# Kernel optimization log

Measured on AMD Instinct MI355X. Metric: run time of the kernel, lower is better.

The kernel has to match this reference:

```python
import jax, jax.numpy as jnp
import numpy as np

PAD_ID = 50256  # GPT-J eos token used as pad


def setup_inputs() -> dict:
    key = jax.random.key(0)
    k1, k2, k3, k4 = jax.random.split(key, 4)
    B, S, D = 4, 2048, 4096  # B preference pairs -> 2B rows
    hidden_states = jax.random.normal(k1, (2 * B, S, D), dtype=jnp.float32)
    v_head_w = jax.random.normal(k2, (D,), dtype=jnp.float32) / np.sqrt(D).astype(np.float32)
    # tokens in [1, PAD_ID) so PAD only appears where we place it
    chosen = jax.random.randint(k3, (B, S), 1, PAD_ID)
    rejected = jax.random.randint(k4, (B, S), 1, PAD_ID)
    PROMPT = 512  # shared prompt so divergence_ind > 0
    rejected = rejected.at[:, :PROMPT].set(chosen[:, :PROMPT])
    pos = jnp.arange(S)[None, :]
    chosen = jnp.where(pos >= 1536, PAD_ID, chosen)     # chosen padded from 1536
    rejected = jnp.where(pos >= 1792, PAD_ID, rejected)  # rejected padded from 1792
    input_ids = jnp.concatenate([chosen, rejected], axis=0).astype(jnp.int64)
    return {"hidden_states": hidden_states, "v_head_w": v_head_w, "input_ids": input_ids}


def _first_index(mask, default):
    # index of first True along last axis, else `default`
    return jnp.where(mask.any(axis=-1), jnp.argmax(mask, axis=-1), default)


def reference(hidden_states, v_head_w, input_ids):
    # v_head: Linear(D, 1, bias=False) then squeeze(-1)
    rewards = jnp.einsum('bsd,d->bs', hidden_states, v_head_w)  # [2B, S]
    bs = input_ids.shape[0] // 2
    S = input_ids.shape[1]
    chosen, rejected = input_ids[:bs], input_ids[bs:]
    c_rew, r_rew = rewards[:bs], rewards[bs:]

    div_ind = _first_index(chosen != rejected, S)       # first divergence per pair
    c_ind = _first_index(chosen == PAD_ID, S)           # first pad (or S)
    r_ind = _first_index(rejected == PAD_ID, S)
    end_ind = jnp.maximum(c_ind, r_ind)

    pos = jnp.arange(S)[None, :]                         # [1, S]
    mask = (pos >= div_ind[:, None]) & (pos < end_ind[:, None])  # truncation window
    cnt = jnp.maximum(mask.sum(axis=-1), 1).astype(rewards.dtype)

    chosen_mean_scores = jnp.sum(jnp.where(mask, c_rew, 0.0), axis=-1) / cnt
    rejected_mean_scores = jnp.sum(jnp.where(mask, r_rew, 0.0), axis=-1) / cnt
    last = (end_ind - 1)[:, None]
    chosen_end_scores = jnp.take_along_axis(c_rew, last, axis=1)[:, 0]
    rejected_end_scores = jnp.take_along_axis(r_rew, last, axis=1)[:, 0]

    # -log(sigmoid(c - r)) averaged over the truncated window, then over pairs
    per_tok = -jax.nn.log_sigmoid(c_rew - r_rew)
    per_sample = jnp.sum(jnp.where(mask, per_tok, 0.0), axis=-1) / cnt
    loss = per_sample.mean()

    return loss, rewards, chosen_mean_scores, rejected_mean_scores, chosen_end_scores, rejected_end_scores
```

## Files before the change

### kernel.cpp

```cpp
#include <hip/hip_runtime.h>
#include <hip/hip_bf16.h>
#include <math.h>

#define PAD_ID 50256
#define S_LEN 2048
#define B_PAIRS 4
#define D4_C 1024
#define ROWS_PER_WAVE 2

__global__ __launch_bounds__(256) void rewards_kernel(
    const float4* __restrict__ hs,
    const float4* __restrict__ w4,
    float* __restrict__ rew,
    int nrows)
{
    const int wave = threadIdx.x >> 6;
    const int lane = threadIdx.x & 63;
    const int row0 = (blockIdx.x * 4 + wave) * ROWS_PER_WAVE;

    float4 wv[16];
    #pragma unroll
    for (int k = 0; k < 16; ++k)
        wv[k] = w4[lane + 64 * k];

    #pragma unroll
    for (int r = 0; r < ROWS_PER_WAVE; ++r) {
        const int row = row0 + r;
        if (row >= nrows) return;
        const float4* rp = hs + (size_t)row * D4_C;

        float acc0 = 0.0f, acc1 = 0.0f;
        #pragma unroll
        for (int k = 0; k < 16; k += 2) {
            float4 a0 = rp[lane + 64 * k];
            float4 a1 = rp[lane + 64 * (k + 1)];
            acc0 = fmaf(a0.x, wv[k].x, acc0);
            acc0 = fmaf(a0.y, wv[k].y, acc0);
            acc0 = fmaf(a0.z, wv[k].z, acc0);
            acc0 = fmaf(a0.w, wv[k].w, acc0);
            acc1 = fmaf(a1.x, wv[k + 1].x, acc1);
            acc1 = fmaf(a1.y, wv[k + 1].y, acc1);
            acc1 = fmaf(a1.z, wv[k + 1].z, acc1);
            acc1 = fmaf(a1.w, wv[k + 1].w, acc1);
        }
        float acc = acc0 + acc1;

        #pragma unroll
        for (int off = 32; off > 0; off >>= 1)
            acc += __shfl_down(acc, off, 64);
        if (lane == 0) rew[row] = acc;
    }
}

__device__ inline float wave_sum(float v) {
    #pragma unroll
    for (int off = 32; off > 0; off >>= 1) v += __shfl_down(v, off, 64);
    return v;
}
__device__ inline int wave_min(int v) {
    #pragma unroll
    for (int off = 32; off > 0; off >>= 1) v = min(v, __shfl_down(v, off, 64));
    return v;
}

__global__ __launch_bounds__(256) void scores_kernel(
    const float* __restrict__ rew,
    const int*   __restrict__ ids,
    float* __restrict__ out)
{
    __shared__ int   si[3][4];
    __shared__ float sf[3][4];
    __shared__ int   s_div, s_end;
    __shared__ float s_loss;

    const int tid  = threadIdx.x;
    const int lane = tid & 63;
    const int wave = tid >> 6;

    if (tid == 0) s_loss = 0.0f;
    __syncthreads();

    for (int b = 0; b < B_PAIRS; ++b) {
        const int*   ch = ids + (size_t)b * S_LEN;
        const int*   rj = ids + (size_t)(B_PAIRS + b) * S_LEN;
        const float* cr = rew + (size_t)b * S_LEN;
        const float* rr = rew + (size_t)(B_PAIRS + b) * S_LEN;

        int ldiv = S_LEN, lc = S_LEN, lr = S_LEN;
        for (int s = tid; s < S_LEN; s += 256) {
            int c = ch[s], r = rj[s];
            if (c != r)      ldiv = min(ldiv, s);
            if (c == PAD_ID) lc   = min(lc, s);
            if (r == PAD_ID) lr   = min(lr, s);
        }
        ldiv = wave_min(ldiv); lc = wave_min(lc); lr = wave_min(lr);
        if (lane == 0) { si[0][wave] = ldiv; si[1][wave] = lc; si[2][wave] = lr; }
        __syncthreads();
        if (tid == 0) {
            int dv = min(min(si[0][0], si[0][1]), min(si[0][2], si[0][3]));
            int ci = min(min(si[1][0], si[1][1]), min(si[1][2], si[1][3]));
            int ri = min(min(si[2][0], si[2][1]), min(si[2][2], si[2][3]));
            s_div = dv;
            s_end = max(ci, ri);
        }
        __syncthreads();
        const int dv = s_div, en = s_end;

        float sc = 0.0f, sr = 0.0f, sl = 0.0f;
        for (int s = dv + tid; s < en; s += 256) {
            float cv = cr[s], rv = rr[s];
            sc += cv;
            sr += rv;
            float x = cv - rv;
            sl += fmaxf(-x, 0.0f) + log1pf(expf(-fabsf(x)));
        }
        sc = wave_sum(sc); sr = wave_sum(sr); sl = wave_sum(sl);
        if (lane == 0) { sf[0][wave] = sc; sf[1][wave] = sr; sf[2][wave] = sl; }
        __syncthreads();
        if (tid == 0) {
            float tsc = sf[0][0] + sf[0][1] + sf[0][2] + sf[0][3];
            float tsr = sf[1][0] + sf[1][1] + sf[1][2] + sf[1][3];
            float tsl = sf[2][0] + sf[2][1] + sf[2][2] + sf[2][3];
            int cnt_i = en - dv;
            if (cnt_i < 1) cnt_i = 1;
            float inv_cnt = 1.0f / (float)cnt_i;
            int last = en - 1;
            if (last < 0) last = 0;
            const int base = 1 + 2 * B_PAIRS * S_LEN;
            out[base + 0 * B_PAIRS + b] = tsc * inv_cnt;
            out[base + 1 * B_PAIRS + b] = tsr * inv_cnt;
            out[base + 2 * B_PAIRS + b] = cr[last];
            out[base + 3 * B_PAIRS + b] = rr[last];
            s_loss += tsl * inv_cnt;
        }
        __syncthreads();
    }
    if (tid == 0) out[0] = s_loss / (float)B_PAIRS;
}

extern "C" void kernel_launch(void* const* d_in, const int* in_sizes, int n_in,
                              void* d_out, int out_size, void* d_ws, size_t ws_size,
                              hipStream_t stream) {
    const float* hs  = (const float*)d_in[0];
    const float* w   = (const float*)d_in[1];
    const int*   ids = (const int*)d_in[2];

    float* out = (float*)d_out;
    float* rew = out + 1;

    const int nrows = in_sizes[0] / in_sizes[1];

    const int rows_per_block = 4 * ROWS_PER_WAVE;
    const int blocks = (nrows + rows_per_block - 1) / rows_per_block;
    rewards_kernel<<<blocks, 256, 0, stream>>>(
        (const float4*)hs, (const float4*)w, rew, nrows);

    scores_kernel<<<1, 256, 0, stream>>>(rew, ids, out);
}
```

Measured before the change: 380.7 us.

## Use nontemporal loads for hidden states and parallelize scores across pairs

The reward dot-product kernel now streams hidden states with nontemporal loads, which is meant to avoid polluting cache with data that is read only once. The scores kernel moves from one 256-thread block looping over pairs to one 1024-thread block per pair. The loss is combined with an atomicAdd into out[0], which the first kernel zeroes. This shortens the serial tail of the scores stage but makes the loss summation order nondeterministic.

```diff
diff --git a/kernel.cpp b/kernel.cpp
--- a/kernel.cpp
+++ b/kernel.cpp
@@ -1,5 +1,4 @@
 #include <hip/hip_runtime.h>
-#include <hip/hip_bf16.h>
 #include <math.h>
 
 #define PAD_ID 50256
@@ -8,17 +7,22 @@
 #define D4_C 1024
 #define ROWS_PER_WAVE 2
 
+typedef float fvec4 __attribute__((ext_vector_type(4)));
+
 __global__ __launch_bounds__(256) void rewards_kernel(
-    const float4* __restrict__ hs,
-    const float4* __restrict__ w4,
-    float* __restrict__ rew,
+    const fvec4* __restrict__ hs,
+    const fvec4* __restrict__ w4,
+    float* __restrict__ out,
     int nrows)
 {
+    if (blockIdx.x == 0 && threadIdx.x == 0) out[0] = 0.0f;
+    float* __restrict__ rew = out + 1;
+
     const int wave = threadIdx.x >> 6;
     const int lane = threadIdx.x & 63;
     const int row0 = (blockIdx.x * 4 + wave) * ROWS_PER_WAVE;
 
-    float4 wv[16];
+    fvec4 wv[16];
     #pragma unroll
     for (int k = 0; k < 16; ++k)
         wv[k] = w4[lane + 64 * k];
@@ -27,13 +31,13 @@
     for (int r = 0; r < ROWS_PER_WAVE; ++r) {
         const int row = row0 + r;
         if (row >= nrows) return;
-        const float4* rp = hs + (size_t)row * D4_C;
+        const fvec4* rp = hs + (size_t)row * D4_C;
 
         float acc0 = 0.0f, acc1 = 0.0f;
         #pragma unroll
         for (int k = 0; k < 16; k += 2) {
-            float4 a0 = rp[lane + 64 * k];
-            float4 a1 = rp[lane + 64 * (k + 1)];
+            fvec4 a0 = __builtin_nontemporal_load(rp + lane + 64 * k);
+            fvec4 a1 = __builtin_nontemporal_load(rp + lane + 64 * (k + 1));
             acc0 = fmaf(a0.x, wv[k].x, acc0);
             acc0 = fmaf(a0.y, wv[k].y, acc0);
             acc0 = fmaf(a0.z, wv[k].z, acc0);
@@ -63,79 +67,78 @@
     return v;
 }
 
-__global__ __launch_bounds__(256) void scores_kernel(
+__global__ __launch_bounds__(1024) void scores_kernel(
     const float* __restrict__ rew,
     const int*   __restrict__ ids,
     float* __restrict__ out)
 {
-    __shared__ int   si[3][4];
-    __shared__ float sf[3][4];
+    __shared__ int   si[3][16];
+    __shared__ float sf[3][16];
     __shared__ int   s_div, s_end;
-    __shared__ float s_loss;
 
+    const int b    = blockIdx.x;
     const int tid  = threadIdx.x;
     const int lane = tid & 63;
     const int wave = tid >> 6;
 
-    if (tid == 0) s_loss = 0.0f;
+    const int*   ch = ids + (size_t)b * S_LEN;
+    const int*   rj = ids + (size_t)(B_PAIRS + b) * S_LEN;
+    const float* cr = rew + (size_t)b * S_LEN;
+    const float* rr = rew + (size_t)(B_PAIRS + b) * S_LEN;
+
+    int ldiv = S_LEN, lc = S_LEN, lr = S_LEN;
+    for (int s = tid; s < S_LEN; s += 1024) {
+        int c = ch[s], r = rj[s];
+        if (c != r)      ldiv = min(ldiv, s);
+        if (c == PAD_ID) lc   = min(lc, s);
+        if (r == PAD_ID) lr   = min(lr, s);
+    }
+    ldiv = wave_min(ldiv); lc = wave_min(lc); lr = wave_min(lr);
+    if (lane == 0) { si[0][wave] = ldiv; si[1][wave] = lc; si[2][wave] = lr; }
     __syncthreads();
+    if (tid == 0) {
+        int dv = S_LEN, ci = S_LEN, ri = S_LEN;
+        #pragma unroll
+        for (int w = 0; w < 16; ++w) {
+            dv = min(dv, si[0][w]);
+            ci = min(ci, si[1][w]);
+            ri = min(ri, si[2][w]);
+        }
+        s_div = dv;
+        s_end = max(ci, ri);
+    }
+    __syncthreads();
+    const int dv = s_div, en = s_end;
 
-    for (int b = 0; b < B_PAIRS; ++b) {
-        const int*   ch = ids + (size_t)b * S_LEN;
-        const int*   rj = ids + (size_t)(B_PAIRS + b) * S_LEN;
-        const float* cr = rew + (size_t)b * S_LEN;
-        const float* rr = rew + (size_t)(B_PAIRS + b) * S_LEN;
-
-        int ldiv = S_LEN, lc = S_LEN, lr = S_LEN;
-        for (int s = tid; s < S_LEN; s += 256) {
-            int c = ch[s], r = rj[s];
-            if (c != r)      ldiv = min(ldiv, s);
-            if (c == PAD_ID) lc   = min(lc, s);
-            if (r == PAD_ID) lr   = min(lr, s);
+    float sc = 0.0f, sr = 0.0f, sl = 0.0f;
+    for (int s = dv + tid; s < en; s += 1024) {
+        float cv = cr[s], rv = rr[s];
+        sc += cv;
+        sr += rv;
+        float x = cv - rv;
+        sl += fmaxf(-x, 0.0f) + log1pf(expf(-fabsf(x)));
+    }
+    sc = wave_sum(sc); sr = wave_sum(sr); sl = wave_sum(sl);
+    if (lane == 0) { sf[0][wave] = sc; sf[1][wave] = sr; sf[2][wave] = sl; }
+    __syncthreads();
+    if (tid == 0) {
+        float tsc = 0.0f, tsr = 0.0f, tsl = 0.0f;
+        #pragma unroll
+        for (int w = 0; w < 16; ++w) {
+            tsc += sf[0][w]; tsr += sf[1][w]; tsl += sf[2][w];
         }
-        ldiv = wave_min(ldiv); lc = wave_min(lc); lr = wave_min(lr);
-        if (lane == 0) { si[0][wave] = ldiv; si[1][wave] = lc; si[2][wave] = lr; }
-        __syncthreads();
-        if (tid == 0) {
-            int dv = min(min(si[0][0], si[0][1]), min(si[0][2], si[0][3]));
-            int ci = min(min(si[1][0], si[1][1]), min(si[1][2], si[1][3]));
-            int ri = min(min(si[2][0], si[2][1]), min(si[2][2], si[2][3]));
-            s_div = dv;
-            s_end = max(ci, ri);
-        }
-        __syncthreads();
-        const int dv = s_div, en = s_end;
-
-        float sc = 0.0f, sr = 0.0f, sl = 0.0f;
-        for (int s = dv + tid; s < en; s += 256) {
-            float cv = cr[s], rv = rr[s];
-            sc += cv;
-            sr += rv;
-            float x = cv - rv;
-            sl += fmaxf(-x, 0.0f) + log1pf(expf(-fabsf(x)));
-        }
-        sc = wave_sum(sc); sr = wave_sum(sr); sl = wave_sum(sl);
-        if (lane == 0) { sf[0][wave] = sc; sf[1][wave] = sr; sf[2][wave] = sl; }
-        __syncthreads();
-        if (tid == 0) {
-            float tsc = sf[0][0] + sf[0][1] + sf[0][2] + sf[0][3];
-            float tsr = sf[1][0] + sf[1][1] + sf[1][2] + sf[1][3];
-            float tsl = sf[2][0] + sf[2][1] + sf[2][2] + sf[2][3];
-            int cnt_i = en - dv;
-            if (cnt_i < 1) cnt_i = 1;
-            float inv_cnt = 1.0f / (float)cnt_i;
-            int last = en - 1;
-            if (last < 0) last = 0;
-            const int base = 1 + 2 * B_PAIRS * S_LEN;
-            out[base + 0 * B_PAIRS + b] = tsc * inv_cnt;
-            out[base + 1 * B_PAIRS + b] = tsr * inv_cnt;
-            out[base + 2 * B_PAIRS + b] = cr[last];
-            out[base + 3 * B_PAIRS + b] = rr[last];
-            s_loss += tsl * inv_cnt;
-        }
-        __syncthreads();
+        int cnt_i = en - dv;
+        if (cnt_i < 1) cnt_i = 1;
+        float inv_cnt = 1.0f / (float)cnt_i;
+        int last = en - 1;
+        if (last < 0) last = 0;
+        const int base = 1 + 2 * B_PAIRS * S_LEN;
+        out[base + 0 * B_PAIRS + b] = tsc * inv_cnt;
+        out[base + 1 * B_PAIRS + b] = tsr * inv_cnt;
+        out[base + 2 * B_PAIRS + b] = cr[last];
+        out[base + 3 * B_PAIRS + b] = rr[last];
+        atomicAdd(out, tsl * inv_cnt * (1.0f / (float)B_PAIRS));
     }
-    if (tid == 0) out[0] = s_loss / (float)B_PAIRS;
 }
 
 extern "C" void kernel_launch(void* const* d_in, const int* in_sizes, int n_in,
@@ -153,7 +156,7 @@
     const int rows_per_block = 4 * ROWS_PER_WAVE;
     const int blocks = (nrows + rows_per_block - 1) / rows_per_block;
     rewards_kernel<<<blocks, 256, 0, stream>>>(
-        (const float4*)hs, (const float4*)w, rew, nrows);
+        (const fvec4*)hs, (const fvec4*)w, out, nrows);
 
-    scores_kernel<<<1, 256, 0, stream>>>(rew, ids, out);
+    scores_kernel<<<B_PAIRS, 1024, 0, stream>>>(rew, ids, out);
 }
```

After: 336.0 us. 11.8% less time.
